# Kernel tuning notes

Hardware: AMD Instinct MI355X
Metric: run time of the kernel (lower is better)

The kernel has to match this reference:

```python
import jax, jax.numpy as jnp
import numpy as np

NUM_USER = 100000
NUM_ENT = 100000
NUM_REL = 60
NUM_ITEM = 20000
ITEM_NUM_IN_KG = 20000
DIM = 64
N_NEIGHBOR = 8
N_ITER = 2
BATCH = 16384


def setup_inputs() -> dict:
    key = jax.random.key(0)
    ks = jax.random.split(key, 10)
    return {
        "u": jax.random.randint(ks[0], (BATCH,), 0, NUM_USER),
        "v": jax.random.randint(ks[1], (BATCH,), 0, NUM_ITEM),
        "usr_emb": jax.random.normal(ks[2], (NUM_USER, DIM), jnp.float32),
        "item_emb": jax.random.normal(ks[3], (NUM_ITEM, DIM), jnp.float32),
        "ent_emb": jax.random.normal(ks[4], (NUM_ENT + 1, DIM), jnp.float32),
        "rel_emb": jax.random.normal(ks[5], (NUM_REL + 1, DIM), jnp.float32),
        "W": jax.random.normal(ks[6], (DIM, DIM), jnp.float32) / np.sqrt(DIM),
        "b": jax.random.normal(ks[7], (DIM,), jnp.float32) * 0.01,
        "adj_ent": jax.random.randint(ks[8], (NUM_ENT + 1, N_NEIGHBOR), 0, NUM_ENT + 1),
        "adj_rel": jax.random.randint(ks[9], (NUM_ENT + 1, N_NEIGHBOR), 0, NUM_REL + 1),
    }


def reference(u, v, usr_emb, item_emb, ent_emb, rel_emb, W, b, adj_ent, adj_rel):
    B = u.shape[0]
    ue = usr_emb[u]  # [B, D]

    # hop-0 indices: items not in the KG map to the padding entity for neighbor lookup
    v_clip = jnp.where(v >= ITEM_NUM_IN_KG, NUM_ENT, v)
    ents = [v_clip[:, None]]  # [B, 1]
    rels = []
    for h in range(N_ITER):
        rels.append(adj_rel[ents[h]].reshape(B, -1))  # [B, 8**(h+1)]
        ents.append(adj_ent[ents[h]].reshape(B, -1))

    # hop-0 embedding uses the ORIGINAL v via the item table (entities[0][:] = v)
    ev = [item_emb[v[:, None]]] + [ent_emb[e] for e in ents[1:]]  # each [B, m, D]
    rv = [rel_emb[r] for r in rels]

    for i in range(N_ITER):
        act = jnp.tanh if i == N_ITER - 1 else jax.nn.sigmoid
        nxt = []
        for hop in range(N_ITER - i):
            sv = ev[hop]  # [B, m, D]
            m = sv.shape[1]
            nv = ev[hop + 1].reshape(B, m, N_NEIGHBOR, DIM)
            nr = rv[hop].reshape(B, m, N_NEIGHBOR, DIM)
            # user-relation attention over the 8 sampled neighbors
            scores = jnp.einsum("bd,bmnd->bmn", ue, nr)
            wgt = jax.nn.softmax(scores, axis=-1)
            agg = jnp.einsum("bmn,bmnd->bmd", wgt, nv)
            out = (sv + agg) @ W.T + b  # 'sum' aggregator
            nxt.append(act(out))
        ev = nxt

    item_vec = ev[0].reshape(B, DIM)
    return jax.nn.sigmoid(jnp.sum(ue * item_vec, axis=1))  # [B]
```

## Files before the change

### kernel.cpp

```cpp
#include <hip/hip_runtime.h>
#include <hip/hip_fp16.h>


namespace {

constexpr int kDim      = 64;
constexpr int kNN       = 8;
constexpr int kNumEnt   = 100000;
constexpr int kItemInKG = 20000;
constexpr int kElems    = 8;
constexpr int kVecs     = 9;
constexpr int kRelChunks = 976;
constexpr size_t kEntHalfBytes = (size_t)(kNumEnt + 1) * kDim * sizeof(__half);

typedef float v2f __attribute__((ext_vector_type(2)));

__device__ __forceinline__ float fast_sigmoid(float x) {
  return 1.0f / (1.0f + __expf(-x));
}
__device__ __forceinline__ float fast_tanh(float x) {
  return 2.0f / (1.0f + __expf(-2.0f * x)) - 1.0f;
}
__device__ __forceinline__ float readlane_f(float v, int lane) {
  return __int_as_float(__builtin_amdgcn_readlane(__float_as_int(v), lane));
}
__device__ __forceinline__ void pk_fma(v2f& acc, v2f a, v2f b) {
  asm("v_pk_fma_f32 %0, %1, %2, %0" : "+v"(acc) : "v"(a), "v"(b));
}

__global__ void __launch_bounds__(256)
conv_kernel(const float* __restrict__ src, __half2* __restrict__ dst, int n4) {
  const int i = blockIdx.x * 256 + threadIdx.x;
  if (i < n4) {
    const float4 f = reinterpret_cast<const float4*>(src)[i];
    dst[2 * i + 0] = __floats2half2_rn(f.x, f.y);
    dst[2 * i + 1] = __floats2half2_rn(f.z, f.w);
  }
}

template <bool HALF>
__global__ void __launch_bounds__(kElems * 64)
__attribute__((amdgpu_waves_per_eu(4, 4)))
kgcn_kernel(const int* __restrict__ u, const int* __restrict__ v,
            const float* __restrict__ usr_emb, const float* __restrict__ item_emb,
            const float* __restrict__ ent_emb, const __half* __restrict__ ent_h,
            const float* __restrict__ rel_emb,
            const float* __restrict__ W, const float* __restrict__ bias,
            const int* __restrict__ adj_ent, const int* __restrict__ adj_rel,
            float* __restrict__ out)
{
  const int tid = threadIdx.x;
  const int wv  = tid >> 6;
  const int ln  = tid & 63;
  const int b   = blockIdx.x * kElems + wv;

  __shared__ float4 s_w4[kDim * 16];
  __shared__ float  s_relt[kDim * 65];
  __shared__ __align__(16) float s_pre[kElems][kVecs][kDim];

  const float4* W4 = reinterpret_cast<const float4*>(W);
  const float4* R4 = reinterpret_cast<const float4*>(rel_emb);
  const float4 wst0 = W4[tid];
  const float4 wst1 = W4[512 + tid];
  const float4 rst0 = R4[tid];
  const float4 rst1 = (512 + tid < kRelChunks) ? R4[512 + tid]
                                               : make_float4(0.f, 0.f, 0.f, 0.f);

  const int   uid = u[b];
  const int   vid = v[b];
  const float ue  = usr_emb[(size_t)uid * kDim + ln];
  const float ev0 = item_emb[(size_t)vid * kDim + ln];
  const int   e0  = (vid >= kItemInKG) ? kNumEnt : vid;

  int e1v = 0, r1v = 0;
  if (ln < kNN) {
    e1v = adj_ent[(size_t)e0 * kNN + ln];
    r1v = adj_rel[(size_t)e0 * kNN + ln];
  }
  const int parent = __shfl(e1v, ln >> 3, 64);
  const int e2v    = adj_ent[(size_t)parent * kNN + (ln & 7)];
  const int r2v    = adj_rel[(size_t)parent * kNN + (ln & 7)];

  {
    int id = tid, row = id >> 4, col = id & 15;
    s_w4[(row << 4) | (col & 8) | ((col ^ row) & 7)] = wst0;
    id = 512 + tid; row = id >> 4; col = id & 15;
    s_w4[(row << 4) | (col & 8) | ((col ^ row) & 7)] = wst1;
  }
  {
    int id = tid, r = id >> 4, c = (id & 15) << 2;
    s_relt[(c + 0) * 65 + r] = rst0.x;
    s_relt[(c + 1) * 65 + r] = rst0.y;
    s_relt[(c + 2) * 65 + r] = rst0.z;
    s_relt[(c + 3) * 65 + r] = rst0.w;
    id = 512 + tid; r = id >> 4; c = (id & 15) << 2;
    s_relt[(c + 0) * 65 + r] = rst1.x;
    s_relt[(c + 1) * 65 + r] = rst1.y;
    s_relt[(c + 2) * 65 + r] = rst1.z;
    s_relt[(c + 3) * 65 + r] = rst1.w;
  }

  float ev1r[kNN];
  #pragma unroll
  for (int m = 0; m < kNN; ++m) {
    const size_t row = (size_t)__builtin_amdgcn_readlane(e1v, m) * kDim + ln;
    ev1r[m] = HALF ? __half2float(ent_h[row]) : ent_emb[row];
  }

  unsigned int g16[kDim];
  if constexpr (HALF) {
    const unsigned short* eh = reinterpret_cast<const unsigned short*>(ent_h);
    #pragma unroll
    for (int i = 0; i < kDim; ++i) {
      const size_t row = (size_t)__builtin_amdgcn_readlane(e2v, i) * kDim + ln;
      g16[i] = eh[row];
    }
  }

  __syncthreads();

  float t;
  {
    const float* relc = &s_relt[ln];
    float a0 = 0.f, a1 = 0.f, a2 = 0.f, a3 = 0.f;
    #pragma unroll
    for (int k = 0; k < kDim; k += 4) {
      a0 = fmaf(readlane_f(ue, k + 0), relc[(k + 0) * 65], a0);
      a1 = fmaf(readlane_f(ue, k + 1), relc[(k + 1) * 65], a1);
      a2 = fmaf(readlane_f(ue, k + 2), relc[(k + 2) * 65], a2);
      a3 = fmaf(readlane_f(ue, k + 3), relc[(k + 3) * 65], a3);
    }
    t = (a0 + a1) + (a2 + a3);
  }

  float w2v;
  {
    const float s2 = __shfl(t, r2v, 64);
    float mx = s2;
    #pragma unroll
    for (int m = 1; m <= 4; m <<= 1) mx = fmaxf(mx, __shfl_xor(mx, m, 64));
    const float e = __expf(s2 - mx);
    float sm = e;
    #pragma unroll
    for (int m = 1; m <= 4; m <<= 1) sm += __shfl_xor(sm, m, 64);
    w2v = e / sm;
  }
  float w0v;
  {
    const float s0 = __shfl(t, r1v, 64);
    float mx = s0;
    #pragma unroll
    for (int m = 1; m <= 4; m <<= 1) mx = fmaxf(mx, __shfl_xor(mx, m, 64));
    w0v = __expf(s0 - mx);
    float sm = w0v;
    #pragma unroll
    for (int m = 1; m <= 4; m <<= 1) sm += __shfl_xor(sm, m, 64);
    w0v /= sm;
  }

  if constexpr (HALF) {
    #pragma unroll
    for (int i = 0; i < kDim; ++i) asm volatile("" : "+v"(g16[i]));
  }

  {
    float agg = 0.f;
    #pragma unroll
    for (int n = 0; n < kNN; ++n)
      agg = fmaf(readlane_f(w0v, n), ev1r[n], agg);
    s_pre[wv][0][ln] = ev0 + agg;
  }
  if constexpr (HALF) {
    #pragma unroll
    for (int m = 0; m < kNN; ++m) {
      float acc = 0.f;
      #pragma unroll
      for (int n = 0; n < kNN; ++n) {
        const float g = __half2float(
            __ushort_as_half((unsigned short)g16[m * kNN + n]));
        acc = fmaf(readlane_f(w2v, m * kNN + n), g, acc);
      }
      s_pre[wv][1 + m][ln] = ev1r[m] + acc;
    }
  } else {
    #pragma unroll 2
    for (int m = 0; m < kNN; ++m) {
      float acc = 0.f;
      #pragma unroll
      for (int n = 0; n < kNN; ++n) {
        const size_t row =
            (size_t)__builtin_amdgcn_readlane(e2v, m * kNN + n) * kDim + ln;
        acc = fmaf(readlane_f(w2v, m * kNN + n), ent_emb[row], acc);
      }
      s_pre[wv][1 + m][ln] = ev1r[m] + acc;
    }
  }

  v2f Wp[32];
  #pragma unroll
  for (int k4 = 0; k4 < 16; ++k4) {
    const float4 wq = s_w4[(ln << 4) | (k4 & 8) | ((k4 ^ ln) & 7)];
    Wp[2 * k4 + 0] = v2f{wq.x, wq.y};
    Wp[2 * k4 + 1] = v2f{wq.z, wq.w};
  }
  #pragma unroll
  for (int i = 0; i < 32; ++i) asm volatile("" : "+v"(Wp[i]));

  const float bln = bias[ln];

  float h[kVecs];
  #pragma unroll
  for (int m = 0; m < kVecs; ++m) {
    const float* p0 = &s_pre[wv][m][0];
    v2f acc01 = v2f{0.f, 0.f}, acc23 = v2f{0.f, 0.f};
    #pragma unroll
    for (int q = 0; q < 16; ++q) {
      const float4 p = *reinterpret_cast<const float4*>(p0 + (q << 2));
      pk_fma(acc01, Wp[2 * q + 0], v2f{p.x, p.y});
      pk_fma(acc23, Wp[2 * q + 1], v2f{p.z, p.w});
    }
    h[m] = fast_sigmoid((acc01.x + acc01.y) + (acc23.x + acc23.y) + bln);
  }

  {
    float pre = h[0];
    #pragma unroll
    for (int n = 0; n < kNN; ++n)
      pre = fmaf(readlane_f(w0v, n), h[1 + n], pre);
    s_pre[wv][0][ln] = pre;
  }

  {
    const float* p0 = &s_pre[wv][0][0];
    v2f acc01 = v2f{0.f, 0.f}, acc23 = v2f{0.f, 0.f};
    #pragma unroll
    for (int q = 0; q < 16; ++q) {
      const float4 p = *reinterpret_cast<const float4*>(p0 + (q << 2));
      pk_fma(acc01, Wp[2 * q + 0], v2f{p.x, p.y});
      pk_fma(acc23, Wp[2 * q + 1], v2f{p.z, p.w});
    }
    const float item =
        fast_tanh((acc01.x + acc01.y) + (acc23.x + acc23.y) + bln);
    float tt = ue * item;
    #pragma unroll
    for (int off = 32; off > 0; off >>= 1)
      tt += __shfl_xor(tt, off, 64);
    if (ln == 0) out[b] = fast_sigmoid(tt);
  }
}

}

extern "C" void kernel_launch(void* const* d_in, const int* in_sizes, int n_in,
                              void* d_out, int out_size, void* d_ws, size_t ws_size,
                              hipStream_t stream) {
  const int*   u        = (const int*)d_in[0];
  const int*   v        = (const int*)d_in[1];
  const float* usr_emb  = (const float*)d_in[2];
  const float* item_emb = (const float*)d_in[3];
  const float* ent_emb  = (const float*)d_in[4];
  const float* rel_emb  = (const float*)d_in[5];
  const float* W        = (const float*)d_in[6];
  const float* bias     = (const float*)d_in[7];
  const int*   adj_ent  = (const int*)d_in[8];
  const int*   adj_rel  = (const int*)d_in[9];
  float*       out      = (float*)d_out;

  const int B = in_sizes[0];
  dim3 grid(B / kElems), block(kElems * 64);

  const bool use_half = (ws_size >= kEntHalfBytes);
  if (use_half) {
    __half* ent_h = (__half*)d_ws;
    const int n4 = (kNumEnt + 1) * kDim / 4;
    hipLaunchKernelGGL(conv_kernel, dim3((n4 + 255) / 256), dim3(256), 0,
                       stream, ent_emb, (__half2*)ent_h, n4);
    hipLaunchKernelGGL((kgcn_kernel<true>), grid, block, 0, stream,
                       u, v, usr_emb, item_emb, ent_emb, ent_h, rel_emb, W,
                       bias, adj_ent, adj_rel, out);
  } else {
    hipLaunchKernelGGL((kgcn_kernel<false>), grid, block, 0, stream,
                       u, v, usr_emb, item_emb, ent_emb, (const __half*)d_ws,
                       rel_emb, W, bias, adj_ent, adj_rel, out);
  }
}
```

Before: 59.26 us.

## Use fp16 MFMA for per-element W projections instead of packed fp32 FMAs

Stores W and the pre-activation vectors in LDS as fp16 and computes the nine hidden projections and the final projection with 16x16x32 MFMA instructions, replacing per-lane packed fp32 dot products. This removes the large per-lane register copy of W and most of the VALU FMA work. In exchange it adds fp16 rounding of activations and weights and LDS round-trips for the hidden vectors, and it over-reads 16 rows per wave, so some fragment rows belong to neighbouring waves and are wasted.

```diff
diff --git a/kernel.cpp b/kernel.cpp
--- a/kernel.cpp
+++ b/kernel.cpp
@@ -9,11 +9,13 @@
 constexpr int kNumEnt   = 100000;
 constexpr int kItemInKG = 20000;
 constexpr int kElems    = 8;
-constexpr int kVecs     = 9;
 constexpr int kRelChunks = 976;
+constexpr int kP        = 72;
 constexpr size_t kEntHalfBytes = (size_t)(kNumEnt + 1) * kDim * sizeof(__half);
 
-typedef float v2f __attribute__((ext_vector_type(2)));
+typedef _Float16 f16x4 __attribute__((ext_vector_type(4)));
+typedef _Float16 f16x8 __attribute__((ext_vector_type(8)));
+typedef float    f32x4 __attribute__((ext_vector_type(4)));
 
 __device__ __forceinline__ float fast_sigmoid(float x) {
   return 1.0f / (1.0f + __expf(-x));
@@ -24,8 +26,8 @@
 __device__ __forceinline__ float readlane_f(float v, int lane) {
   return __int_as_float(__builtin_amdgcn_readlane(__float_as_int(v), lane));
 }
-__device__ __forceinline__ void pk_fma(v2f& acc, v2f a, v2f b) {
-  asm("v_pk_fma_f32 %0, %1, %2, %0" : "+v"(acc) : "v"(a), "v"(b));
+__device__ __forceinline__ f16x8 join8(f16x4 lo, f16x4 hi) {
+  return __builtin_shufflevector(lo, hi, 0, 1, 2, 3, 4, 5, 6, 7);
 }
 
 __global__ void __launch_bounds__(256)
@@ -52,11 +54,15 @@
   const int tid = threadIdx.x;
   const int wv  = tid >> 6;
   const int ln  = tid & 63;
+  const int lq  = ln & 15;
+  const int lg  = ln >> 4;
   const int b   = blockIdx.x * kElems + wv;
 
-  __shared__ float4 s_w4[kDim * 16];
-  __shared__ float  s_relt[kDim * 65];
-  __shared__ __align__(16) float s_pre[kElems][kVecs][kDim];
+  __shared__ _Float16 s_wh[kDim * kP];
+  __shared__ float    s_relt[kDim * 65];
+  __shared__ _Float16 s_pre[80 * kP];
+  __shared__ _Float16 s_h[72 * kP];
+  __shared__ float    s_ue[kElems][kDim];
 
   const float4* W4 = reinterpret_cast<const float4*>(W);
   const float4* R4 = reinterpret_cast<const float4*>(rel_emb);
@@ -82,10 +88,16 @@
   const int r2v    = adj_rel[(size_t)parent * kNN + (ln & 7)];
 
   {
-    int id = tid, row = id >> 4, col = id & 15;
-    s_w4[(row << 4) | (col & 8) | ((col ^ row) & 7)] = wst0;
-    id = 512 + tid; row = id >> 4; col = id & 15;
-    s_w4[(row << 4) | (col & 8) | ((col ^ row) & 7)] = wst1;
+    int id = tid, row = id >> 4, c4 = (id & 15) << 2;
+    f16x4 h4;
+    h4[0] = (_Float16)wst0.x; h4[1] = (_Float16)wst0.y;
+    h4[2] = (_Float16)wst0.z; h4[3] = (_Float16)wst0.w;
+    *reinterpret_cast<f16x4*>(&s_wh[row * kP + c4]) = h4;
+    id = 512 + tid; row = id >> 4; c4 = (id & 15) << 2;
+    f16x4 h5;
+    h5[0] = (_Float16)wst1.x; h5[1] = (_Float16)wst1.y;
+    h5[2] = (_Float16)wst1.z; h5[3] = (_Float16)wst1.w;
+    *reinterpret_cast<f16x4*>(&s_wh[row * kP + c4]) = h5;
   }
   {
     int id = tid, r = id >> 4, c = (id & 15) << 2;
@@ -99,6 +111,7 @@
     s_relt[(c + 2) * 65 + r] = rst1.z;
     s_relt[(c + 3) * 65 + r] = rst1.w;
   }
+  s_ue[wv][ln] = ue;
 
   float ev1r[kNN];
   #pragma unroll
@@ -168,7 +181,7 @@
     #pragma unroll
     for (int n = 0; n < kNN; ++n)
       agg = fmaf(readlane_f(w0v, n), ev1r[n], agg);
-    s_pre[wv][0][ln] = ev0 + agg;
+    s_pre[(wv * 9 + 0) * kP + ln] = (_Float16)(ev0 + agg);
   }
   if constexpr (HALF) {
     #pragma unroll
@@ -180,7 +193,7 @@
             __ushort_as_half((unsigned short)g16[m * kNN + n]));
         acc = fmaf(readlane_f(w2v, m * kNN + n), g, acc);
       }
-      s_pre[wv][1 + m][ln] = ev1r[m] + acc;
+      s_pre[(wv * 9 + 1 + m) * kP + ln] = (_Float16)(ev1r[m] + acc);
     }
   } else {
     #pragma unroll 2
@@ -192,61 +205,91 @@
             (size_t)__builtin_amdgcn_readlane(e2v, m * kNN + n) * kDim + ln;
         acc = fmaf(readlane_f(w2v, m * kNN + n), ent_emb[row], acc);
       }
-      s_pre[wv][1 + m][ln] = ev1r[m] + acc;
-    }
-  }
-
-  v2f Wp[32];
-  #pragma unroll
-  for (int k4 = 0; k4 < 16; ++k4) {
-    const float4 wq = s_w4[(ln << 4) | (k4 & 8) | ((k4 ^ ln) & 7)];
-    Wp[2 * k4 + 0] = v2f{wq.x, wq.y};
-    Wp[2 * k4 + 1] = v2f{wq.z, wq.w};
-  }
-  #pragma unroll
-  for (int i = 0; i < 32; ++i) asm volatile("" : "+v"(Wp[i]));
-
-  const float bln = bias[ln];
-
-  float h[kVecs];
-  #pragma unroll
-  for (int m = 0; m < kVecs; ++m) {
-    const float* p0 = &s_pre[wv][m][0];
-    v2f acc01 = v2f{0.f, 0.f}, acc23 = v2f{0.f, 0.f};
-    #pragma unroll
-    for (int q = 0; q < 16; ++q) {
-      const float4 p = *reinterpret_cast<const float4*>(p0 + (q << 2));
-      pk_fma(acc01, Wp[2 * q + 0], v2f{p.x, p.y});
-      pk_fma(acc23, Wp[2 * q + 1], v2f{p.z, p.w});
-    }
-    h[m] = fast_sigmoid((acc01.x + acc01.y) + (acc23.x + acc23.y) + bln);
-  }
-
-  {
-    float pre = h[0];
+      s_pre[(wv * 9 + 1 + m) * kP + ln] = (_Float16)(ev1r[m] + acc);
+    }
+  }
+
+  float bcol[4];
+  #pragma unroll
+  for (int tt = 0; tt < 4; ++tt) bcol[tt] = bias[tt * 16 + lq];
+
+  f16x8 Bf[8];
+  #pragma unroll
+  for (int tt = 0; tt < 4; ++tt) {
+    #pragma unroll
+    for (int s = 0; s < 2; ++s) {
+      const _Float16* p = &s_wh[(tt * 16 + lq) * kP + s * 32 + lg * 4];
+      Bf[tt * 2 + s] = join8(*reinterpret_cast<const f16x4*>(p),
+                             *reinterpret_cast<const f16x4*>(p + 16));
+    }
+  }
+
+  f16x8 Af[2];
+  #pragma unroll
+  for (int s = 0; s < 2; ++s) {
+    const _Float16* p = &s_pre[(wv * 9 + lq) * kP + s * 32 + lg * 4];
+    Af[s] = join8(*reinterpret_cast<const f16x4*>(p),
+                  *reinterpret_cast<const f16x4*>(p + 16));
+  }
+  f32x4 acc[4];
+  #pragma unroll
+  for (int tt = 0; tt < 4; ++tt) acc[tt] = f32x4{0.f, 0.f, 0.f, 0.f};
+  #pragma unroll
+  for (int tt = 0; tt < 4; ++tt)
+    #pragma unroll
+    for (int s = 0; s < 2; ++s)
+      acc[tt] = __builtin_amdgcn_mfma_f32_16x16x32_f16(Af[s], Bf[tt * 2 + s],
+                                                       acc[tt], 0, 0, 0);
+
+  #pragma unroll
+  for (int tt = 0; tt < 4; ++tt) {
+    #pragma unroll
+    for (int r = 0; r < 4; ++r) {
+      const int vec = lg * 4 + r;
+      if (vec < 9)
+        s_h[(wv * 9 + vec) * kP + tt * 16 + lq] =
+            (_Float16)fast_sigmoid(acc[tt][r] + bcol[tt]);
+    }
+  }
+
+  {
+    float pre = (float)s_h[(wv * 9 + 0) * kP + ln];
     #pragma unroll
     for (int n = 0; n < kNN; ++n)
-      pre = fmaf(readlane_f(w0v, n), h[1 + n], pre);
-    s_pre[wv][0][ln] = pre;
-  }
-
-  {
-    const float* p0 = &s_pre[wv][0][0];
-    v2f acc01 = v2f{0.f, 0.f}, acc23 = v2f{0.f, 0.f};
-    #pragma unroll
-    for (int q = 0; q < 16; ++q) {
-      const float4 p = *reinterpret_cast<const float4*>(p0 + (q << 2));
-      pk_fma(acc01, Wp[2 * q + 0], v2f{p.x, p.y});
-      pk_fma(acc23, Wp[2 * q + 1], v2f{p.z, p.w});
-    }
-    const float item =
-        fast_tanh((acc01.x + acc01.y) + (acc23.x + acc23.y) + bln);
-    float tt = ue * item;
-    #pragma unroll
-    for (int off = 32; off > 0; off >>= 1)
-      tt += __shfl_xor(tt, off, 64);
-    if (ln == 0) out[b] = fast_sigmoid(tt);
-  }
+      pre = fmaf(readlane_f(w0v, n), (float)s_h[(wv * 9 + 1 + n) * kP + ln],
+                 pre);
+    s_pre[(wv * 9 + 0) * kP + ln] = (_Float16)pre;
+  }
+
+  f16x8 Ff[2];
+  #pragma unroll
+  for (int s = 0; s < 2; ++s) {
+    const _Float16* p = &s_pre[(wv * 9 + 0) * kP + s * 32 + lg * 4];
+    Ff[s] = join8(*reinterpret_cast<const f16x4*>(p),
+                  *reinterpret_cast<const f16x4*>(p + 16));
+  }
+  f32x4 fa[4];
+  #pragma unroll
+  for (int tt = 0; tt < 4; ++tt) fa[tt] = f32x4{0.f, 0.f, 0.f, 0.f};
+  #pragma unroll
+  for (int tt = 0; tt < 4; ++tt)
+    #pragma unroll
+    for (int s = 0; s < 2; ++s)
+      fa[tt] = __builtin_amdgcn_mfma_f32_16x16x32_f16(Ff[s], Bf[tt * 2 + s],
+                                                      fa[tt], 0, 0, 0);
+
+  float part = 0.f;
+  if (ln < 16) {
+    #pragma unroll
+    for (int tt = 0; tt < 4; ++tt) {
+      const float item = fast_tanh(fa[tt][0] + bcol[tt]);
+      part = fmaf(item, s_ue[wv][tt * 16 + ln], part);
+    }
+  }
+  #pragma unroll
+  for (int off = 1; off <= 8; off <<= 1)
+    part += __shfl_xor(part, off, 64);
+  if (ln == 0) out[b] = fast_sigmoid(part);
 }
 
 }
```

New measurement: 53.38 us. -9.9%, faster.
